# Kernel optimization log

Measured on AMD Instinct MI355X. Metric: run time of the kernel, lower is better.

## Reference

```python
import jax, jax.numpy as jnp
import numpy as np
from jax import lax

# ---- config (matches init_kwargs) ----
B, T, H = 4, 2048, 1024
HU = 4 * H                 # h_up = hidden*4
LAYERS, INDEX = 12, 0
K_CLAMP, K_EPS = 60.0, 1e-8
LN_EPS = 1e-5


def setup_inputs() -> dict:
    key = jax.random.key(0)
    ks = jax.random.split(key, 9)
    s = 0.02  # weight scale
    tr01 = INDEX / (LAYERS - 1)          # time_ratio_0_to_1
    tr1pz = 1.0 - INDEX / LAYERS         # time_ratio_1_to_pz
    i_h = np.arange(H, dtype=np.float64) / H
    i_hu = np.arange(HU, dtype=np.float64)
    # per-channel decay speed / first (sized to the WKV channel dim h_up)
    decay_speed = -5.0 + 8.0 * (i_hu / (HU - 1)) ** (0.7 + 1.3 * tr01)
    zigzag = ((np.arange(HU) + 1) % 3 - 1) * 0.5
    time_first = np.log(0.3) + zigzag
    f32 = lambda a: jnp.asarray(a, jnp.float32)
    return {
        "x": jax.random.normal(ks[0], (B, T, H), jnp.float32),
        "ln0_g": jnp.ones((H,), jnp.float32), "ln0_b": jnp.zeros((H,), jnp.float32),
        "pre_g": jnp.ones((H,), jnp.float32), "pre_b": jnp.zeros((H,), jnp.float32),
        "post_g": jnp.ones((H,), jnp.float32), "post_b": jnp.zeros((H,), jnp.float32),
        "tm_decay": f32(decay_speed),
        "tm_first": f32(time_first),
        "tm_mix_k": f32(i_h ** tr1pz),
        "tm_mix_v": f32(i_h ** tr1pz + 0.3 * tr01),
        "tm_mix_r": f32(i_h ** (0.5 * tr1pz)),
        "tm_Wk": jax.random.normal(ks[1], (H, HU), jnp.float32) * s,
        "tm_Wv": jax.random.normal(ks[2], (H, HU), jnp.float32) * s,
        "tm_Wr": jax.random.normal(ks[3], (H, HU), jnp.float32) * s,
        "tm_Wo": jax.random.normal(ks[4], (HU, H), jnp.float32) * s,
        "cm_mix_k": f32(i_h ** tr1pz),
        "cm_mix_r": f32(i_h ** tr1pz),
        "cm_Wk": jax.random.normal(ks[5], (H, HU), jnp.float32) * s,
        "cm_Wv": jax.random.normal(ks[6], (HU, H), jnp.float32) * s,
        "cm_Wr": jax.random.normal(ks[7], (H, H), jnp.float32) * s,
    }


def _ln(x, g, b):
    m = jnp.mean(x, -1, keepdims=True)
    v = jnp.mean((x - m) ** 2, -1, keepdims=True)
    return (x - m) / jnp.sqrt(v + LN_EPS) * g + b


def _shift(x):  # ZeroPad2d((0,0,1,-1)): xx[:, t] = x[:, t-1], xx[:, 0] = 0
    return jnp.pad(x[:, :-1], ((0, 0), (1, 0), (0, 0)))


def _wkv(k, kv, decay, first):
    # k, kv: [B, T, HU]; decay, first: [HU]
    # wkv[t] = first*kv[t] + sum_{d>=1} decay^(d-1) * kv[t-d]  (same for k)
    def step(carry, inp):
        sk, skv = carry
        kt, kvt = inp
        out = (first * kt + sk, first * kvt + skv)
        return (kt + decay * sk, kvt + decay * skv), out
    b = k.shape[0]
    init = (jnp.zeros((b, k.shape[2]), k.dtype), jnp.zeros((b, k.shape[2]), k.dtype))
    _, (wk, wkv) = lax.scan(step, init, (jnp.swapaxes(k, 0, 1), jnp.swapaxes(kv, 0, 1)))
    return jnp.swapaxes(wk, 0, 1), jnp.swapaxes(wkv, 0, 1)


def reference(x, ln0_g, ln0_b, pre_g, pre_b, post_g, post_b,
              tm_decay, tm_first, tm_mix_k, tm_mix_v, tm_mix_r,
              tm_Wk, tm_Wv, tm_Wr, tm_Wo,
              cm_mix_k, cm_mix_r, cm_Wk, cm_Wv, cm_Wr):
    if INDEX == 0:
        x = _ln(x, ln0_g, ln0_b)

    # ---- RWKV_TM (time mix / WKV) ----
    xn = _ln(x, pre_g, pre_b)
    xx = _shift(xn)
    xk = xn * tm_mix_k + xx * (1.0 - tm_mix_k)
    xv = xn * tm_mix_v + xx * (1.0 - tm_mix_v)
    xr = xn * tm_mix_r + xx * (1.0 - tm_mix_r)
    k = jnp.exp(jnp.minimum(xk @ tm_Wk, K_CLAMP))   # [B,T,HU]
    v = xv @ tm_Wv                                  # [B,T,HU]
    r = xr @ tm_Wr                                  # [B,T,HU]
    kv = k * v
    decay = jnp.exp(-jnp.exp(tm_decay))  # per-step multiplier exp(-exp(time_decay))
    first = jnp.exp(tm_first)
    wk, wkv = _wkv(k, kv, decay, first)
    rwkv = jax.nn.sigmoid(r) * (wkv / (wk + K_EPS))
    x = x + rwkv @ tm_Wo

    # ---- RWKV_CM (channel mix) ----
    xn = _ln(x, post_g, post_b)
    xx = _shift(xn)
    xk = xn * cm_mix_k + xx * (1.0 - cm_mix_k)
    xr = xn * cm_mix_r + xx * (1.0 - cm_mix_r)
    kv = jax.nn.silu(xk @ cm_Wk) @ cm_Wv            # [B,T,H]
    x = x + (jax.nn.sigmoid(xr @ cm_Wr) + kv)
    return x
```

## Files before the change

### kernel.cpp

```cpp
#include <hip/hip_runtime.h>

#define Hdim  1024
#define Tdim  2048
#define Bdim  4
#define HUdim 4096
#define Mrows (Bdim*Tdim)
#define CHUNK 2048
#define NCH   (HUdim/CHUNK)
#define NSEG  16
#define SEGL  (Tdim/NSEG)
#define SCHUNK 16

typedef __bf16 bf16;
typedef __bf16 bf16x2 __attribute__((ext_vector_type(2)));
typedef __bf16 bf16x8 __attribute__((ext_vector_type(8)));
typedef float  floatx4 __attribute__((ext_vector_type(4)));

__device__ __forceinline__ bf16 f2bf(float x) { return (bf16)x; }

__global__ __launch_bounds__(256) void wconv_all(
    const float* __restrict__ s0, const float* __restrict__ s1, const float* __restrict__ s2,
    const float* __restrict__ s3, const float* __restrict__ s4, const float* __restrict__ s5,
    const float* __restrict__ s6,
    bf16* d0, bf16* d1, bf16* d2, bf16* d3, bf16* d4, bf16* d5, bf16* d6) {
  __shared__ float tile[64][65];
  int bid = blockIdx.x;
  const float* src; bf16* dst; int K, N, local;
  if (bid < 1024)      { src = s0; dst = d0; K = Hdim;  N = HUdim; local = bid; }
  else if (bid < 2048) { src = s1; dst = d1; K = Hdim;  N = HUdim; local = bid - 1024; }
  else if (bid < 3072) { src = s2; dst = d2; K = Hdim;  N = HUdim; local = bid - 2048; }
  else if (bid < 4096) { src = s3; dst = d3; K = HUdim; N = Hdim;  local = bid - 3072; }
  else if (bid < 5120) { src = s4; dst = d4; K = Hdim;  N = HUdim; local = bid - 4096; }
  else if (bid < 6144) { src = s5; dst = d5; K = HUdim; N = Hdim;  local = bid - 5120; }
  else                 { src = s6; dst = d6; K = Hdim;  N = Hdim;  local = bid - 6144; }
  const int nt = N >> 6;
  const int n0 = (local % nt) * 64, k0 = (local / nt) * 64;
  const int tr = threadIdx.x >> 6;
  const int tc = threadIdx.x & 63;
#pragma unroll
  for (int j = 0; j < 16; j++) {
    int r = j * 4 + tr;
    tile[r][tc] = src[(size_t)(k0 + r) * N + n0 + tc];
  }
  __syncthreads();
#pragma unroll
  for (int j = 0; j < 16; j++) {
    int r = j * 4 + tr;
    dst[(size_t)(n0 + r) * K + k0 + tc] = f2bf(tile[tc][r]);
  }
}

__device__ __forceinline__ void block_reduce4(float v[4], float* sm) {
#pragma unroll
  for (int off = 32; off > 0; off >>= 1) {
#pragma unroll
    for (int i = 0; i < 4; i++) v[i] += __shfl_down(v[i], off, 64);
  }
  const int w = threadIdx.x >> 6;
  if ((threadIdx.x & 63) == 0) {
#pragma unroll
    for (int i = 0; i < 4; i++) sm[w * 4 + i] = v[i];
  }
  __syncthreads();
#pragma unroll
  for (int i = 0; i < 4; i++) v[i] = sm[i] + sm[4 + i] + sm[8 + i] + sm[12 + i];
  __syncthreads();
}

__global__ __launch_bounds__(256) void ln_mix_tm(
    const float* __restrict__ x,
    const float* __restrict__ g0, const float* __restrict__ b0,
    const float* __restrict__ g1, const float* __restrict__ b1,
    const float* __restrict__ mk, const float* __restrict__ mv, const float* __restrict__ mr,
    float* __restrict__ x0, bf16* __restrict__ xk, bf16* __restrict__ xv, bf16* __restrict__ xr) {
  __shared__ float sm[16];
  const int bid = blockIdx.x;
  const int t = bid & (Tdim - 1);
  const int tid = threadIdx.x;
  const bool havep = (t > 0);
  const float hp = havep ? 1.f : 0.f;
  const float* rowc = x + (size_t)bid * Hdim;
  const float* rowp = havep ? (rowc - Hdim) : rowc;

  float c[4], p[4];
#pragma unroll
  for (int j = 0; j < 4; j++) c[j] = rowc[tid * 4 + j];
#pragma unroll
  for (int j = 0; j < 4; j++) p[j] = rowp[tid * 4 + j] * hp;

  float red[4] = {0.f, 0.f, 0.f, 0.f};
#pragma unroll
  for (int j = 0; j < 4; j++) { red[0] += c[j]; red[1] += c[j]*c[j]; red[2] += p[j]; red[3] += p[j]*p[j]; }
  block_reduce4(red, sm);
  const float inv = 1.f / Hdim;
  float mc = red[0]*inv, vc = red[1]*inv - mc*mc;
  float mp = red[2]*inv, vp = red[3]*inv - mp*mp;
  float sc = rsqrtf(vc + 1e-5f), sp = rsqrtf(vp + 1e-5f);

  float yc[4], yp[4];
#pragma unroll
  for (int j = 0; j < 4; j++) {
    int i = tid * 4 + j;
    yc[j] = (c[j] - mc) * sc * g0[i] + b0[i];
    yp[j] = ((p[j] - mp) * sp * g0[i] + b0[i]) * hp;
    x0[(size_t)bid * Hdim + i] = yc[j];
  }

  float r2[4] = {0.f, 0.f, 0.f, 0.f};
#pragma unroll
  for (int j = 0; j < 4; j++) { r2[0] += yc[j]; r2[1] += yc[j]*yc[j]; r2[2] += yp[j]; r2[3] += yp[j]*yp[j]; }
  block_reduce4(r2, sm);
  float mc2 = r2[0]*inv, vc2 = r2[1]*inv - mc2*mc2;
  float mp2 = r2[2]*inv, vp2 = r2[3]*inv - mp2*mp2;
  float sc2 = rsqrtf(vc2 + 1e-5f), sp2 = rsqrtf(vp2 + 1e-5f);

#pragma unroll
  for (int j = 0; j < 4; j++) {
    int i = tid * 4 + j;
    float xnc = (yc[j] - mc2) * sc2 * g1[i] + b1[i];
    float xnp = ((yp[j] - mp2) * sp2 * g1[i] + b1[i]) * hp;
    size_t o = (size_t)bid * Hdim + i;
    float a;
    a = mk[i]; xk[o] = f2bf(xnc * a + xnp * (1.f - a));
    a = mv[i]; xv[o] = f2bf(xnc * a + xnp * (1.f - a));
    a = mr[i]; xr[o] = f2bf(xnc * a + xnp * (1.f - a));
  }
}

__global__ __launch_bounds__(256) void ln_mix_cm(
    const float* __restrict__ xin,
    const float* __restrict__ g, const float* __restrict__ bb,
    const float* __restrict__ mk, const float* __restrict__ mr,
    bf16* __restrict__ xk, bf16* __restrict__ xr) {
  __shared__ float sm[16];
  const int bid = blockIdx.x;
  const int t = bid & (Tdim - 1);
  const int tid = threadIdx.x;
  const bool havep = (t > 0);
  const float hp = havep ? 1.f : 0.f;
  const float* rowc = xin + (size_t)bid * Hdim;
  const float* rowp = havep ? (rowc - Hdim) : rowc;

  float c[4], p[4];
#pragma unroll
  for (int j = 0; j < 4; j++) c[j] = rowc[tid * 4 + j];
#pragma unroll
  for (int j = 0; j < 4; j++) p[j] = rowp[tid * 4 + j] * hp;

  float red[4] = {0.f, 0.f, 0.f, 0.f};
#pragma unroll
  for (int j = 0; j < 4; j++) { red[0] += c[j]; red[1] += c[j]*c[j]; red[2] += p[j]; red[3] += p[j]*p[j]; }
  block_reduce4(red, sm);
  const float inv = 1.f / Hdim;
  float mc = red[0]*inv, vc = red[1]*inv - mc*mc;
  float mp = red[2]*inv, vp = red[3]*inv - mp*mp;
  float sc = rsqrtf(vc + 1e-5f), sp = rsqrtf(vp + 1e-5f);

#pragma unroll
  for (int j = 0; j < 4; j++) {
    int i = tid * 4 + j;
    float xnc = (c[j] - mc) * sc * g[i] + bb[i];
    float xnp = ((p[j] - mp) * sp * g[i] + bb[i]) * hp;
    size_t o = (size_t)bid * Hdim + i;
    float a;
    a = mk[i]; xk[o] = f2bf(xnc * a + xnp * (1.f - a));
    a = mr[i]; xr[o] = f2bf(xnc * a + xnp * (1.f - a));
  }
}

__global__ __launch_bounds__(64) void wkv_part(
    const bf16* __restrict__ Kb, const bf16* __restrict__ Vb,
    float* __restrict__ stK, float* __restrict__ stKV,
    const float* __restrict__ tdec) {
  const int seg = blockIdx.x & (NSEG - 1);
  const int rest = blockIdx.x >> 4;
  const int b = rest >> 4, g = rest & 15;
  const int c = (g << 7) + (threadIdx.x << 1);
  const float d0 = __expf(-__expf(tdec[c]));
  const float d1 = __expf(-__expf(tdec[c + 1]));
  size_t base = ((size_t)b * Tdim + (size_t)seg * SEGL) * CHUNK + c;
  float sk0 = 0.f, skv0 = 0.f, sk1 = 0.f, skv1 = 0.f;
  for (int t0 = 0; t0 < SEGL; t0 += SCHUNK) {
    bf16x2 kk[SCHUNK], vv[SCHUNK];
#pragma unroll
    for (int j = 0; j < SCHUNK; j++) {
      size_t idx = base + (size_t)(t0 + j) * CHUNK;
      kk[j] = *(const bf16x2*)(Kb + idx);
      vv[j] = *(const bf16x2*)(Vb + idx);
    }
#pragma unroll
    for (int j = 0; j < SCHUNK; j++) {
      float k0 = (float)kk[j][0], k1 = (float)kk[j][1];
      float v0 = (float)vv[j][0], v1 = (float)vv[j][1];
      sk0  = fmaf(d0, sk0, k0);   skv0 = fmaf(d0, skv0, k0 * v0);
      sk1  = fmaf(d1, sk1, k1);   skv1 = fmaf(d1, skv1, k1 * v1);
    }
  }
  size_t so = ((size_t)seg * Bdim + b) * CHUNK + c;
  stK[so]      = sk0;  stK[so + 1]  = sk1;
  stKV[so]     = skv0; stKV[so + 1] = skv1;
}

__global__ __launch_bounds__(64) void wkv_emit(
    const bf16* __restrict__ Kb, const bf16* __restrict__ Vb,
    const bf16* SRb, bf16* Pb,
    const float* __restrict__ stK, const float* __restrict__ stKV,
    const float* __restrict__ tdec, const float* __restrict__ tfst) {
  const int seg = blockIdx.x & (NSEG - 1);
  const int rest = blockIdx.x >> 4;
  const int b = rest >> 4, g = rest & 15;
  const int c = (g << 7) + (threadIdx.x << 1);
  const float ed0 = __expf(tdec[c]),     ed1 = __expf(tdec[c + 1]);
  const float d0  = __expf(-ed0),        d1  = __expf(-ed1);
  const float df0 = __expf(-ed0 * (float)SEGL);
  const float df1 = __expf(-ed1 * (float)SEGL);
  const float f0  = __expf(tfst[c]),     f1  = __expf(tfst[c + 1]);

  float sk0 = 0.f, skv0 = 0.f, sk1 = 0.f, skv1 = 0.f;
  for (int j = 0; j < seg; j++) {
    size_t so = ((size_t)j * Bdim + b) * CHUNK + c;
    sk0  = fmaf(df0, sk0,  stK[so]);      sk1  = fmaf(df1, sk1,  stK[so + 1]);
    skv0 = fmaf(df0, skv0, stKV[so]);     skv1 = fmaf(df1, skv1, stKV[so + 1]);
  }

  size_t base = ((size_t)b * Tdim + (size_t)seg * SEGL) * CHUNK + c;
  for (int t0 = 0; t0 < SEGL; t0 += SCHUNK) {
    bf16x2 kk[SCHUNK], vv[SCHUNK], rr[SCHUNK];
#pragma unroll
    for (int j = 0; j < SCHUNK; j++) {
      size_t idx = base + (size_t)(t0 + j) * CHUNK;
      kk[j] = *(const bf16x2*)(Kb + idx);
      vv[j] = *(const bf16x2*)(Vb + idx);
      rr[j] = *(const bf16x2*)(SRb + idx);
    }
#pragma unroll
    for (int j = 0; j < SCHUNK; j++) {
      size_t idx = base + (size_t)(t0 + j) * CHUNK;
      float k0 = (float)kk[j][0], k1 = (float)kk[j][1];
      float v0 = (float)vv[j][0], v1 = (float)vv[j][1];
      float kv0 = k0 * v0, kv1 = k1 * v1;
      float wk0  = fmaf(f0, k0, sk0) + 1e-8f;
      float wk1  = fmaf(f1, k1, sk1) + 1e-8f;
      float wkv0 = fmaf(f0, kv0, skv0);
      float wkv1 = fmaf(f1, kv1, skv1);
      bf16x2 out;
      out[0] = f2bf((float)rr[j][0] * wkv0 * __builtin_amdgcn_rcpf(wk0));
      out[1] = f2bf((float)rr[j][1] * wkv1 * __builtin_amdgcn_rcpf(wk1));
      *(bf16x2*)(Pb + idx) = out;
      sk0  = fmaf(d0, sk0, k0);   skv0 = fmaf(d0, skv0, kv0);
      sk1  = fmaf(d1, sk1, k1);   skv1 = fmaf(d1, skv1, kv1);
    }
  }
}

__device__ __forceinline__ void gld_lds(const bf16* g, bf16* l) {
  __builtin_amdgcn_global_load_lds(
      (const __attribute__((address_space(1))) void*)(g),
      (__attribute__((address_space(3))) void*)(l),
      16, 0, 0);
}

__device__ __forceinline__ void swz(int s, int gm, int& m_t, int& n_t) {
  const int mpx  = gm >> 3;
  const int xcd  = s & 7;
  const int ss   = s >> 3;
  const int pass = mpx << 1;
  const int ng   = ss / pass;
  const int rem  = ss - ng * pass;
  m_t = xcd * mpx + (rem >> 1);
  n_t = (ng << 1) + (rem & 1);
}

__device__ __forceinline__ void mm_core64(
    const bf16* A, const bf16* Bt, int lda, int ldb, int K,
    long m0, long n0, int wv, int lane, int wm, int wn,
    bf16* As, bf16* Bs, floatx4 acc[4][4]) {
  const int srow = wv * 32 + (lane >> 2);
  const int scol = (((lane & 3) - ((lane >> 3) & 3)) & 3) * 8;
  const bf16* gA = A + (m0 + srow) * (long)lda + scol;
  const bf16* gB = Bt + (n0 + srow) * (long)ldb + scol;
  const long skipA = 16L * lda;
  const long skipB = 16L * ldb;
  bf16* lA = As + wv * 1024;
  bf16* lB = Bs + wv * 1024;
  const int pg = ((lane >> 4) + ((lane >> 1) & 3)) & 3;
  const bf16* fa = As + ((wm * 64) + (lane & 15)) * 32 + pg * 8;
  const bf16* fb = Bs + ((wn * 64) + (lane & 15)) * 32 + pg * 8;

  const int ksteps = K >> 6;
  for (int kt = 0; kt < ksteps; ++kt) {
    __syncthreads();
    gld_lds(gA, lA);             gld_lds(gA + skipA, lA + 512);
    gld_lds(gA + 32, lA + 4096); gld_lds(gA + 32 + skipA, lA + 4096 + 512);
    gld_lds(gB, lB);             gld_lds(gB + skipB, lB + 512);
    gld_lds(gB + 32, lB + 4096); gld_lds(gB + 32 + skipB, lB + 4096 + 512);
    gA += 64; gB += 64;
    __syncthreads();
#pragma unroll
    for (int s = 0; s < 2; s++) {
      bf16x8 af[4], bfr[4];
#pragma unroll
      for (int i = 0; i < 4; i++) {
        af[i]  = *(const bf16x8*)(fa + s * 4096 + i * 512);
        bfr[i] = *(const bf16x8*)(fb + s * 4096 + i * 512);
      }
#pragma unroll
      for (int mt = 0; mt < 4; mt++)
#pragma unroll
        for (int nt = 0; nt < 4; nt++)
          acc[mt][nt] = __builtin_amdgcn_mfma_f32_16x16x32_bf16(af[mt], bfr[nt], acc[mt][nt], 0, 0, 0);
    }
  }
}

enum { E_EXP = 0, E_BF16 = 1, E_SIG = 2, E_ADD1 = 3, E_SILU = 4, E_F32 = 5, E_SIGADD2 = 6 };

template <int EPI>
__device__ __forceinline__ void epilogue(
    floatx4 acc[4][4], void* Cout, const void* aux1, const void* aux2,
    long m0, long n0, int ldc, int lane, int wm, int wn) {
  const int r0 = wm * 64 + ((lane >> 4) << 2);
  const int c0 = wn * 64 + (lane & 15);
#pragma unroll
  for (int mt = 0; mt < 4; mt++) {
#pragma unroll
    for (int i = 0; i < 4; i++) {
      long r = m0 + r0 + mt * 16 + i;
      long bidx = r * (long)ldc + n0 + c0;
#pragma unroll
      for (int nt = 0; nt < 4; nt++) {
        long idx = bidx + nt * 16;
        float v = acc[mt][nt][i];
        if constexpr (EPI == E_EXP) {
          ((bf16*)Cout)[idx] = f2bf(__expf(fminf(v, 60.f)));
        } else if constexpr (EPI == E_BF16) {
          ((bf16*)Cout)[idx] = f2bf(v);
        } else if constexpr (EPI == E_SIG) {
          ((bf16*)Cout)[idx] = f2bf(1.f / (1.f + __expf(-v)));
        } else if constexpr (EPI == E_ADD1) {
          float prev = ((const float*)aux1)[idx];
          ((float*)Cout)[idx] = v + prev;
        } else if constexpr (EPI == E_SILU) {
          ((bf16*)Cout)[idx] = f2bf(v / (1.f + __expf(-v)));
        } else if constexpr (EPI == E_F32) {
          ((float*)Cout)[idx] = v;
        } else {
          float a1 = ((const float*)aux1)[idx];
          float a2 = ((const float*)aux2)[idx];
          ((float*)Cout)[idx] = a1 + 1.f / (1.f + __expf(-v)) + a2;
        }
      }
    }
  }
}

template <int EPI, int MT>
__global__ __launch_bounds__(256) void gemm_bt(
    const bf16* __restrict__ A, const bf16* __restrict__ Bt,
    void* Cout, const void* aux1, const void* aux2,
    int lda, int ldb, int ldc, int K, int gm, int gn) {
  __shared__ __align__(16) bf16 As[2 * 128 * 32];
  __shared__ __align__(16) bf16 Bs[2 * 128 * 32];
  const int tid = threadIdx.x;
  const int lane = tid & 63;
  const int wv = tid >> 6;
  const int wm = wv >> 1, wn = wv & 1;
  int m_t, n_t;
  swz(blockIdx.x, gm, m_t, n_t);
  const long n0 = (long)n_t * 128;

#pragma unroll
  for (int sm = 0; sm < MT; sm++) {
    const long m0 = (long)m_t * (128 * MT) + sm * 128;
    floatx4 acc[4][4];
#pragma unroll
    for (int i = 0; i < 4; i++)
#pragma unroll
      for (int j = 0; j < 4; j++) acc[i][j] = (floatx4){0.f, 0.f, 0.f, 0.f};
    mm_core64(A, Bt, lda, ldb, K, m0, n0, wv, lane, wm, wn, As, Bs, acc);
    epilogue<EPI>(acc, Cout, aux1, aux2, m0, n0, ldc, lane, wm, wn);
  }
}

__global__ __launch_bounds__(256) void proj3(
    const bf16* __restrict__ xk, const bf16* __restrict__ xv, const bf16* __restrict__ xr,
    const bf16* __restrict__ Wk, const bf16* __restrict__ Wv, const bf16* __restrict__ Wr,
    bf16* Kc, bf16* Vc, bf16* SRc, int gm, int gn) {
  __shared__ __align__(16) bf16 As[2 * 128 * 32];
  __shared__ __align__(16) bf16 Bs[2 * 128 * 32];
  const int per = gm * gn;
  const int sub = blockIdx.x / per;
  const int s   = blockIdx.x - sub * per;
  const int tid = threadIdx.x;
  const int lane = tid & 63;
  const int wv = tid >> 6;
  const int wm = wv >> 1, wn = wv & 1;
  int m_t, n_t;
  swz(s, gm, m_t, n_t);
  const long n0 = (long)n_t * 128;

  const bf16* A  = (sub == 0) ? xk : (sub == 1) ? xv : xr;
  const bf16* Bt = (sub == 0) ? Wk : (sub == 1) ? Wv : Wr;
  bf16*       C  = (sub == 0) ? Kc : (sub == 1) ? Vc : SRc;

#pragma unroll
  for (int sm = 0; sm < 2; sm++) {
    const long m0 = (long)m_t * 256 + sm * 128;
    floatx4 acc[4][4];
#pragma unroll
    for (int i = 0; i < 4; i++)
#pragma unroll
      for (int j = 0; j < 4; j++) acc[i][j] = (floatx4){0.f, 0.f, 0.f, 0.f};
    mm_core64(A, Bt, Hdim, Hdim, Hdim, m0, n0, wv, lane, wm, wn, As, Bs, acc);

    const int r0 = wm * 64 + ((lane >> 4) << 2);
    const int c0 = wn * 64 + (lane & 15);
#pragma unroll
    for (int mt = 0; mt < 4; mt++) {
#pragma unroll
      for (int i = 0; i < 4; i++) {
        long r = m0 + r0 + mt * 16 + i;
        long bidx = r * (long)CHUNK + n0 + c0;
#pragma unroll
        for (int nt = 0; nt < 4; nt++) {
          long idx = bidx + nt * 16;
          float v = acc[mt][nt][i];
          float o;
          if (sub == 0)      o = __expf(fminf(v, 60.f));
          else if (sub == 1) o = v;
          else               o = 1.f / (1.f + __expf(-v));
          C[idx] = f2bf(o);
        }
      }
    }
  }
}

extern "C" void kernel_launch(void* const* d_in, const int* in_sizes, int n_in,
                              void* d_out, int out_size, void* d_ws, size_t ws_size,
                              hipStream_t stream) {
  (void)in_sizes; (void)n_in; (void)out_size; (void)ws_size;
  const float* x        = (const float*)d_in[0];
  const float* ln0_g    = (const float*)d_in[1];
  const float* ln0_b    = (const float*)d_in[2];
  const float* pre_g    = (const float*)d_in[3];
  const float* pre_b    = (const float*)d_in[4];
  const float* post_g   = (const float*)d_in[5];
  const float* post_b   = (const float*)d_in[6];
  const float* tm_decay = (const float*)d_in[7];
  const float* tm_first = (const float*)d_in[8];
  const float* tm_mix_k = (const float*)d_in[9];
  const float* tm_mix_v = (const float*)d_in[10];
  const float* tm_mix_r = (const float*)d_in[11];
  const float* tm_Wk    = (const float*)d_in[12];
  const float* tm_Wv    = (const float*)d_in[13];
  const float* tm_Wr    = (const float*)d_in[14];
  const float* tm_Wo    = (const float*)d_in[15];
  const float* cm_mix_k = (const float*)d_in[16];
  const float* cm_mix_r = (const float*)d_in[17];
  const float* cm_Wk    = (const float*)d_in[18];
  const float* cm_Wv    = (const float*)d_in[19];
  const float* cm_Wr    = (const float*)d_in[20];

  char* ws = (char*)d_ws;
  bf16*  WkT  = (bf16*)(ws + 0);
  bf16*  WvT  = (bf16*)(ws + 8388608);
  bf16*  WrT  = (bf16*)(ws + 16777216);
  bf16*  WoT  = (bf16*)(ws + 25165824);
  bf16*  cWkT = (bf16*)(ws + 33554432);
  bf16*  cWvT = (bf16*)(ws + 41943040);
  bf16*  cWrT = (bf16*)(ws + 50331648);
  float* xres = (float*)(ws + 52428800);
  bf16*  xk   = (bf16*)(ws + 85983232);
  bf16*  xv   = (bf16*)(ws + 102760448);
  bf16*  xr   = (bf16*)(ws + 119537664);
  bf16*  Kc   = (bf16*)(ws + 136314880);
  bf16*  Vc   = (bf16*)(ws + 169869312);
  bf16*  SRc  = (bf16*)(ws + 203423744);
  float* stK  = (float*)(ws + 236978176);
  float* stKV = (float*)(ws + 237502464);
  bf16*  xk2  = (bf16*)(ws + 136314880);
  bf16*  xr2  = (bf16*)(ws + 153092096);
  bf16*  hbuf = (bf16*)(ws + 169869312);
  float* hv   = (float*)(ws + 85983232);

  dim3 blk(256);
  wconv_all<<<6400, blk, 0, stream>>>(tm_Wk, tm_Wv, tm_Wr, tm_Wo, cm_Wk, cm_Wv, cm_Wr,
                                      WkT, WvT, WrT, WoT, cWkT, cWvT, cWrT);

  ln_mix_tm<<<Mrows, blk, 0, stream>>>(x, ln0_g, ln0_b, pre_g, pre_b,
                                       tm_mix_k, tm_mix_v, tm_mix_r, xres, xk, xv, xr);

  const int scan_grid = NSEG * Bdim * (CHUNK / 128);
  const int GM = Mrows / 128;
  const int GM2 = Mrows / 256;
  const int GNp = CHUNK / 128;
  for (int ch = 0; ch < NCH; ch++) {
    const long woff = (long)ch * CHUNK;
    proj3<<<3 * GM2 * GNp, blk, 0, stream>>>(
        xk, xv, xr, WkT + woff * Hdim, WvT + woff * Hdim, WrT + woff * Hdim,
        Kc, Vc, SRc, GM2, GNp);

    wkv_part<<<scan_grid, dim3(64), 0, stream>>>(
        Kc, Vc, stK, stKV, tm_decay + woff);
    wkv_emit<<<scan_grid, dim3(64), 0, stream>>>(
        Kc, Vc, SRc, SRc, stK, stKV, tm_decay + woff, tm_first + woff);

    gemm_bt<E_ADD1, 1><<<GM * (Hdim/128), blk, 0, stream>>>(
        SRc, WoT + woff, xres, xres, nullptr, CHUNK, HUdim, Hdim, CHUNK, GM, Hdim/128);
  }

  ln_mix_cm<<<Mrows, blk, 0, stream>>>(xres, post_g, post_b, cm_mix_k, cm_mix_r, xk2, xr2);

  gemm_bt<E_SILU, 2><<<GM2 * (HUdim/128), blk, 0, stream>>>(
      xk2, cWkT, hbuf, nullptr, nullptr, Hdim, Hdim, HUdim, Hdim, GM2, HUdim/128);

  gemm_bt<E_F32, 1><<<GM * (Hdim/128), blk, 0, stream>>>(
      hbuf, cWvT, hv, nullptr, nullptr, HUdim, HUdim, Hdim, CHUNK, GM, Hdim/128);
  gemm_bt<E_ADD1, 1><<<GM * (Hdim/128), blk, 0, stream>>>(
      hbuf + CHUNK, cWvT + CHUNK, hv, hv, nullptr, HUdim, HUdim, Hdim, CHUNK, GM, Hdim/128);

  gemm_bt<E_SIGADD2, 1><<<GM * (Hdim/128), blk, 0, stream>>>(
      xr2, cWrT, (float*)d_out, xres, hv, Hdim, Hdim, Hdim, Hdim, GM, Hdim/128);
}
```

Measured before the change: 988.2 us.

## Use 256x256 eight-wave MFMA GEMM tiles for projections and channel-mix up-proj

Adds a 512-thread GEMM core that computes a 256x256 output tile per block. It uses 128-deep K stages double-buffered in LDS via direct global-to-LDS loads, with phased barriers and setprio around the MFMA bursts. The time-mix projection kernel and the channel-mix SiLU up-projection now use this core in place of the 128-wide, 4-wave tiles. Larger tiles raise arithmetic intensity and cut global and LDS traffic per FLOP, at the cost of higher register and LDS use (128KB LDS per block) and fewer blocks for load balancing.

```diff
diff --git a/kernel.cpp b/kernel.cpp
--- a/kernel.cpp
+++ b/kernel.cpp
@@ -382,55 +382,187 @@
   }
 }
 
-__global__ __launch_bounds__(256) void proj3(
+__device__ __forceinline__ void mm_core256(
+    const bf16* __restrict__ A, const bf16* __restrict__ Bt,
+    int lda, int ldb, int K, long m0, long n0,
+    int wv, int lane, bf16* Lds, floatx4 acc[8][4]) {
+  const int wm = wv >> 2, wn = wv & 3;
+  const int rA0 = wm * 128 + (wv & 3) * 16;
+  const int rB0 = (wv >> 1) * 64 + (wv & 1) * 16;
+  const int rl  = lane >> 2;
+  const int scol = (((lane & 3) - ((lane >> 3) & 3)) & 3) * 8;
+  const bf16* gA = A + (m0 + rA0 + rl) * (long)lda + scol;
+  const bf16* gB = Bt + (n0 + rB0 + rl) * (long)ldb + scol;
+  bf16* lA = Lds + rA0 * 32;
+  bf16* lB = Lds + 16384 + rB0 * 32;
+
+  const int pg = ((lane >> 4) + ((lane >> 1) & 3)) & 3;
+  const bf16* fa0 = Lds + (wm * 128 + (lane & 15)) * 32 + pg * 8;
+  const bf16* fb0 = Lds + 16384 + (wn * 64 + (lane & 15)) * 32 + pg * 8;
+
+#define STGA8(buf, h, kt) do { \
+    const bf16* _s = gA + (long)(h) * 64 * lda + (kt) * 64; \
+    bf16* _d = lA + (buf) * 32768 + (h) * 2048; \
+    gld_lds(_s, _d); gld_lds(_s + 32, _d + 8192); } while (0)
+#define STGB8(buf, h, kt) do { \
+    const bf16* _s = gB + (long)(h) * 32 * ldb + (kt) * 64; \
+    bf16* _d = lB + (buf) * 32768 + (h) * 1024; \
+    gld_lds(_s, _d); gld_lds(_s + 32, _d + 8192); } while (0)
+
+  STGA8(0, 0, 0); STGA8(0, 1, 0); STGB8(0, 0, 0); STGB8(0, 1, 0);
+  STGA8(1, 0, 1); STGB8(1, 0, 1);
+  asm volatile("s_waitcnt vmcnt(4)" ::: "memory");
+  __builtin_amdgcn_s_barrier();
+
+  const int niter = K >> 7;
+  for (int it = 0; it < niter; ++it) {
+    const int kt0 = it << 1;
+    const bool notlast = (it != niter - 1);
+#pragma unroll
+    for (int ph = 0; ph < 8; ++ph) {
+      const int buf = ph >> 2;
+      const int mq = (ph >> 1) & 1, nq = ph & 1;
+      bf16x8 a[4][2], b[2][2];
+      const bf16* fa = fa0 + buf * 32768 + mq * 2048;
+      const bf16* fb = fb0 + buf * 32768 + nq * 1024;
+#pragma unroll
+      for (int mf = 0; mf < 4; ++mf) {
+        a[mf][0] = *(const bf16x8*)(fa + mf * 512);
+        a[mf][1] = *(const bf16x8*)(fa + mf * 512 + 8192);
+      }
+#pragma unroll
+      for (int nf = 0; nf < 2; ++nf) {
+        b[nf][0] = *(const bf16x8*)(fb + nf * 512);
+        b[nf][1] = *(const bf16x8*)(fb + nf * 512 + 8192);
+      }
+      __builtin_amdgcn_sched_barrier(0);
+      if (ph == 0)      STGA8(1, 1, kt0 + 1);
+      else if (ph == 1) STGB8(1, 1, kt0 + 1);
+      else if (notlast) {
+        if (ph == 2)      STGA8(0, 0, kt0 + 2);
+        else if (ph == 3) STGB8(0, 0, kt0 + 2);
+        else if (ph == 4) STGA8(0, 1, kt0 + 2);
+        else if (ph == 5) STGB8(0, 1, kt0 + 2);
+        else if (ph == 6) STGA8(1, 0, kt0 + 3);
+        else              STGB8(1, 0, kt0 + 3);
+      }
+      if (ph == 3) {
+        if (notlast) { asm volatile("s_waitcnt vmcnt(4)" ::: "memory"); }
+        else         { asm volatile("s_waitcnt vmcnt(0)" ::: "memory"); }
+      } else if (ph == 7 && notlast) {
+        asm volatile("s_waitcnt vmcnt(4)" ::: "memory");
+      }
+      __builtin_amdgcn_s_barrier();
+      asm volatile("s_waitcnt lgkmcnt(0)" ::: "memory");
+      __builtin_amdgcn_s_setprio(1);
+#pragma unroll
+      for (int mf = 0; mf < 4; ++mf)
+#pragma unroll
+        for (int nf = 0; nf < 2; ++nf) {
+          acc[mq*4+mf][nq*2+nf] = __builtin_amdgcn_mfma_f32_16x16x32_bf16(
+              a[mf][0], b[nf][0], acc[mq*4+mf][nq*2+nf], 0, 0, 0);
+          acc[mq*4+mf][nq*2+nf] = __builtin_amdgcn_mfma_f32_16x16x32_bf16(
+              a[mf][1], b[nf][1], acc[mq*4+mf][nq*2+nf], 0, 0, 0);
+        }
+      __builtin_amdgcn_s_setprio(0);
+      __builtin_amdgcn_s_barrier();
+    }
+  }
+#undef STGA8
+#undef STGB8
+}
+
+template <int EPI>
+__global__ __launch_bounds__(512, 2) void gemm8(
+    const bf16* __restrict__ A, const bf16* __restrict__ Bt,
+    void* Cout, const void* aux1, const void* aux2,
+    int lda, int ldb, int ldc, int K, int gm, int gn) {
+  __shared__ __align__(16) bf16 Lds[65536];
+  const int tid = threadIdx.x;
+  const int lane = tid & 63;
+  const int wv = tid >> 6;
+  int m_t, n_t;
+  swz(blockIdx.x, gm, m_t, n_t);
+  const long m0 = (long)m_t * 256, n0 = (long)n_t * 256;
+  floatx4 acc[8][4];
+#pragma unroll
+  for (int i = 0; i < 8; i++)
+#pragma unroll
+    for (int j = 0; j < 4; j++) acc[i][j] = (floatx4){0.f, 0.f, 0.f, 0.f};
+  mm_core256(A, Bt, lda, ldb, K, m0, n0, wv, lane, Lds, acc);
+
+  const int wm = wv >> 2, wn = wv & 3;
+  const int r0 = wm * 128 + ((lane >> 4) << 2);
+  const int c0 = wn * 64 + (lane & 15);
+#pragma unroll
+  for (int mf = 0; mf < 8; ++mf) {
+#pragma unroll
+    for (int i = 0; i < 4; ++i) {
+      long r = m0 + r0 + mf * 16 + i;
+      long bidx = r * (long)ldc + n0 + c0;
+#pragma unroll
+      for (int nf = 0; nf < 4; ++nf) {
+        long idx = bidx + nf * 16;
+        float v = acc[mf][nf][i];
+        if constexpr (EPI == E_SILU) {
+          ((bf16*)Cout)[idx] = f2bf(v / (1.f + __expf(-v)));
+        } else if constexpr (EPI == E_BF16) {
+          ((bf16*)Cout)[idx] = f2bf(v);
+        } else if constexpr (EPI == E_F32) {
+          ((float*)Cout)[idx] = v;
+        } else if constexpr (EPI == E_ADD1) {
+          float prev = ((const float*)aux1)[idx];
+          ((float*)Cout)[idx] = v + prev;
+        }
+      }
+    }
+  }
+}
+
+__global__ __launch_bounds__(512, 2) void proj8(
     const bf16* __restrict__ xk, const bf16* __restrict__ xv, const bf16* __restrict__ xr,
     const bf16* __restrict__ Wk, const bf16* __restrict__ Wv, const bf16* __restrict__ Wr,
     bf16* Kc, bf16* Vc, bf16* SRc, int gm, int gn) {
-  __shared__ __align__(16) bf16 As[2 * 128 * 32];
-  __shared__ __align__(16) bf16 Bs[2 * 128 * 32];
+  __shared__ __align__(16) bf16 Lds[65536];
   const int per = gm * gn;
   const int sub = blockIdx.x / per;
   const int s   = blockIdx.x - sub * per;
   const int tid = threadIdx.x;
   const int lane = tid & 63;
   const int wv = tid >> 6;
-  const int wm = wv >> 1, wn = wv & 1;
   int m_t, n_t;
   swz(s, gm, m_t, n_t);
-  const long n0 = (long)n_t * 128;
+  const long m0 = (long)m_t * 256, n0 = (long)n_t * 256;
 
   const bf16* A  = (sub == 0) ? xk : (sub == 1) ? xv : xr;
   const bf16* Bt = (sub == 0) ? Wk : (sub == 1) ? Wv : Wr;
   bf16*       C  = (sub == 0) ? Kc : (sub == 1) ? Vc : SRc;
 
-#pragma unroll
-  for (int sm = 0; sm < 2; sm++) {
-    const long m0 = (long)m_t * 256 + sm * 128;
-    floatx4 acc[4][4];
-#pragma unroll
-    for (int i = 0; i < 4; i++)
-#pragma unroll
-      for (int j = 0; j < 4; j++) acc[i][j] = (floatx4){0.f, 0.f, 0.f, 0.f};
-    mm_core64(A, Bt, Hdim, Hdim, Hdim, m0, n0, wv, lane, wm, wn, As, Bs, acc);
-
-    const int r0 = wm * 64 + ((lane >> 4) << 2);
-    const int c0 = wn * 64 + (lane & 15);
-#pragma unroll
-    for (int mt = 0; mt < 4; mt++) {
-#pragma unroll
-      for (int i = 0; i < 4; i++) {
-        long r = m0 + r0 + mt * 16 + i;
-        long bidx = r * (long)CHUNK + n0 + c0;
-#pragma unroll
-        for (int nt = 0; nt < 4; nt++) {
-          long idx = bidx + nt * 16;
-          float v = acc[mt][nt][i];
-          float o;
-          if (sub == 0)      o = __expf(fminf(v, 60.f));
-          else if (sub == 1) o = v;
-          else               o = 1.f / (1.f + __expf(-v));
-          C[idx] = f2bf(o);
-        }
+  floatx4 acc[8][4];
+#pragma unroll
+  for (int i = 0; i < 8; i++)
+#pragma unroll
+    for (int j = 0; j < 4; j++) acc[i][j] = (floatx4){0.f, 0.f, 0.f, 0.f};
+  mm_core256(A, Bt, Hdim, Hdim, Hdim, m0, n0, wv, lane, Lds, acc);
+
+  const int wm = wv >> 2, wn = wv & 3;
+  const int r0 = wm * 128 + ((lane >> 4) << 2);
+  const int c0 = wn * 64 + (lane & 15);
+#pragma unroll
+  for (int mf = 0; mf < 8; ++mf) {
+#pragma unroll
+    for (int i = 0; i < 4; ++i) {
+      long r = m0 + r0 + mf * 16 + i;
+      long bidx = r * (long)CHUNK + n0 + c0;
+#pragma unroll
+      for (int nf = 0; nf < 4; ++nf) {
+        long idx = bidx + nf * 16;
+        float v = acc[mf][nf][i];
+        float o;
+        if (sub == 0)      o = __expf(fminf(v, 60.f));
+        else if (sub == 1) o = v;
+        else               o = 1.f / (1.f + __expf(-v));
+        C[idx] = f2bf(o);
       }
     }
   }
@@ -493,13 +625,13 @@
 
   const int scan_grid = NSEG * Bdim * (CHUNK / 128);
   const int GM = Mrows / 128;
-  const int GM2 = Mrows / 256;
-  const int GNp = CHUNK / 128;
+  const int GM8 = Mrows / 256;
+  const int GN8p = CHUNK / 256;
   for (int ch = 0; ch < NCH; ch++) {
     const long woff = (long)ch * CHUNK;
-    proj3<<<3 * GM2 * GNp, blk, 0, stream>>>(
+    proj8<<<3 * GM8 * GN8p, dim3(512), 0, stream>>>(
         xk, xv, xr, WkT + woff * Hdim, WvT + woff * Hdim, WrT + woff * Hdim,
-        Kc, Vc, SRc, GM2, GNp);
+        Kc, Vc, SRc, GM8, GN8p);
 
     wkv_part<<<scan_grid, dim3(64), 0, stream>>>(
         Kc, Vc, stK, stKV, tm_decay + woff);
@@ -512,8 +644,8 @@
 
   ln_mix_cm<<<Mrows, blk, 0, stream>>>(xres, post_g, post_b, cm_mix_k, cm_mix_r, xk2, xr2);
 
-  gemm_bt<E_SILU, 2><<<GM2 * (HUdim/128), blk, 0, stream>>>(
-      xk2, cWkT, hbuf, nullptr, nullptr, Hdim, Hdim, HUdim, Hdim, GM2, HUdim/128);
+  gemm8<E_SILU><<<GM8 * (HUdim/256), dim3(512), 0, stream>>>(
+      xk2, cWkT, hbuf, nullptr, nullptr, Hdim, Hdim, HUdim, Hdim, GM8, HUdim/256);
 
   gemm_bt<E_F32, 1><<<GM * (Hdim/128), blk, 0, stream>>>(
       hbuf, cWvT, hv, nullptr, nullptr, HUdim, HUdim, Hdim, CHUNK, GM, Hdim/128);
```

Result: faster. 926.5 us (-6.2%).

## Replace GEMM core with 8-wave triple-buffered pipelined 256x128 tile kernel

Applied to the files above, without the earlier changes.

Replaces the 4-wave, single-buffered 128x128 GEMM main loop with an 8-wave (512-thread) kernel computing 256x128 tiles. Global-to-LDS loads are staged two k-steps ahead in a triple-buffered LDS ring, with vmcnt waits, s_setprio around the MFMA bursts and a single barrier per iteration, so loads overlap compute. All projection and channel-mix GEMMs switch to the new kernel, and the split-K pair for cm_Wv is merged into one full-K GEMM. The larger LDS footprint and 2-blocks-per-CU launch bound trade occupancy and register headroom for more tile reuse.

```diff
diff --git a/kernel.cpp b/kernel.cpp
--- a/kernel.cpp
+++ b/kernel.cpp
@@ -269,48 +269,6 @@
   const int rem  = ss - ng * pass;
   m_t = xcd * mpx + (rem >> 1);
   n_t = (ng << 1) + (rem & 1);
-}
-
-__device__ __forceinline__ void mm_core64(
-    const bf16* A, const bf16* Bt, int lda, int ldb, int K,
-    long m0, long n0, int wv, int lane, int wm, int wn,
-    bf16* As, bf16* Bs, floatx4 acc[4][4]) {
-  const int srow = wv * 32 + (lane >> 2);
-  const int scol = (((lane & 3) - ((lane >> 3) & 3)) & 3) * 8;
-  const bf16* gA = A + (m0 + srow) * (long)lda + scol;
-  const bf16* gB = Bt + (n0 + srow) * (long)ldb + scol;
-  const long skipA = 16L * lda;
-  const long skipB = 16L * ldb;
-  bf16* lA = As + wv * 1024;
-  bf16* lB = Bs + wv * 1024;
-  const int pg = ((lane >> 4) + ((lane >> 1) & 3)) & 3;
-  const bf16* fa = As + ((wm * 64) + (lane & 15)) * 32 + pg * 8;
-  const bf16* fb = Bs + ((wn * 64) + (lane & 15)) * 32 + pg * 8;
-
-  const int ksteps = K >> 6;
-  for (int kt = 0; kt < ksteps; ++kt) {
-    __syncthreads();
-    gld_lds(gA, lA);             gld_lds(gA + skipA, lA + 512);
-    gld_lds(gA + 32, lA + 4096); gld_lds(gA + 32 + skipA, lA + 4096 + 512);
-    gld_lds(gB, lB);             gld_lds(gB + skipB, lB + 512);
-    gld_lds(gB + 32, lB + 4096); gld_lds(gB + 32 + skipB, lB + 4096 + 512);
-    gA += 64; gB += 64;
-    __syncthreads();
-#pragma unroll
-    for (int s = 0; s < 2; s++) {
-      bf16x8 af[4], bfr[4];
-#pragma unroll
-      for (int i = 0; i < 4; i++) {
-        af[i]  = *(const bf16x8*)(fa + s * 4096 + i * 512);
-        bfr[i] = *(const bf16x8*)(fb + s * 4096 + i * 512);
-      }
-#pragma unroll
-      for (int mt = 0; mt < 4; mt++)
-#pragma unroll
-        for (int nt = 0; nt < 4; nt++)
-          acc[mt][nt] = __builtin_amdgcn_mfma_f32_16x16x32_bf16(af[mt], bfr[nt], acc[mt][nt], 0, 0, 0);
-    }
-  }
 }
 
 enum { E_EXP = 0, E_BF16 = 1, E_SIG = 2, E_ADD1 = 3, E_SILU = 4, E_F32 = 5, E_SIGADD2 = 6 };
@@ -354,83 +312,147 @@
   }
 }
 
-template <int EPI, int MT>
-__global__ __launch_bounds__(256) void gemm_bt(
+__device__ __forceinline__ void mm_core_n128(
+    const bf16* __restrict__ A, const bf16* __restrict__ Bt,
+    int lda, int ldb, int K, long m0, long n0,
+    int wv, int lane, bf16* Lds, floatx4 acc[4][4]) {
+  const int rl  = lane >> 2;
+  const int scol = (((lane & 3) - ((lane >> 3) & 3)) & 3) * 8;
+  const bf16* gA = A + (m0 + wv * 16 + rl) * (long)lda + scol;
+  const bf16* gB = Bt + (n0 + wv * 16 + rl) * (long)ldb + scol;
+  bf16* lA = Lds + wv * 512;
+  bf16* lB = Lds + 49152 + wv * 512;
+
+  const int wm = wv >> 1, wn = wv & 1;
+  const int pg = ((lane >> 4) + ((lane >> 1) & 3)) & 3;
+  const bf16* fa0 = Lds + (wm * 64 + (lane & 15)) * 32 + pg * 8;
+  const bf16* fb0 = Lds + 49152 + (wn * 64 + (lane & 15)) * 32 + pg * 8;
+
+#define STGA_N(buf, h, kt) do { \
+    const bf16* _s = gA + (long)(h) * 128 * lda + (long)(kt) * 64; \
+    bf16* _d = lA + (buf) * 16384 + (h) * 4096; \
+    gld_lds(_s, _d); gld_lds(_s + 32, _d + 8192); } while (0)
+#define STGB_N(buf, kt) do { \
+    const bf16* _s = gB + (long)(kt) * 64; \
+    bf16* _d = lB + (buf) * 8192; \
+    gld_lds(_s, _d); gld_lds(_s + 32, _d + 4096); } while (0)
+
+  STGA_N(0, 0, 0); STGA_N(0, 1, 0); STGB_N(0, 0);
+  STGA_N(1, 0, 1); STGA_N(1, 1, 1); STGB_N(1, 1);
+  asm volatile("s_waitcnt vmcnt(6)" ::: "memory");
+  __builtin_amdgcn_s_barrier();
+
+  const int niter = K >> 6;
+  int p = 0;
+  for (int it = 0; it < niter; ++it) {
+    const int q = (p >= 1) ? p - 1 : p + 2;
+    const bool dostage = (it <= niter - 3);
+    const bf16* fa = fa0 + p * 16384;
+    const bf16* fb = fb0 + p * 8192;
+
+    bf16x8 a0[4], b0v[4], a1[4], b1v[4];
+#pragma unroll
+    for (int i = 0; i < 4; ++i) {
+      a0[i]  = *(const bf16x8*)(fa + i * 512);
+      b0v[i] = *(const bf16x8*)(fb + i * 512);
+    }
+#pragma unroll
+    for (int i = 0; i < 4; ++i) {
+      a1[i]  = *(const bf16x8*)(fa + 8192 + i * 512);
+      b1v[i] = *(const bf16x8*)(fb + 4096 + i * 512);
+    }
+    __builtin_amdgcn_sched_barrier(0);
+    if (dostage) { STGA_N(q, 0, it + 2); STGA_N(q, 1, it + 2); STGB_N(q, it + 2); }
+    __builtin_amdgcn_s_setprio(1);
+#pragma unroll
+    for (int mf = 0; mf < 4; ++mf)
+#pragma unroll
+      for (int nf = 0; nf < 4; ++nf)
+        acc[mf][nf] = __builtin_amdgcn_mfma_f32_16x16x32_bf16(a0[mf], b0v[nf], acc[mf][nf], 0, 0, 0);
+#pragma unroll
+    for (int mf = 0; mf < 4; ++mf)
+#pragma unroll
+      for (int nf = 0; nf < 4; ++nf)
+        acc[mf][nf] = __builtin_amdgcn_mfma_f32_16x16x32_bf16(a1[mf], b1v[nf], acc[mf][nf], 0, 0, 0);
+    __builtin_amdgcn_s_setprio(0);
+
+    if (it < niter - 1) {
+      if (dostage) asm volatile("s_waitcnt vmcnt(6)" ::: "memory");
+      else         asm volatile("s_waitcnt vmcnt(0)" ::: "memory");
+      __builtin_amdgcn_s_barrier();
+    }
+    p = (p == 2) ? 0 : p + 1;
+  }
+#undef STGA_N
+#undef STGB_N
+}
+
+template <int EPI>
+__global__ __launch_bounds__(512, 2) void gemm8n(
     const bf16* __restrict__ A, const bf16* __restrict__ Bt,
     void* Cout, const void* aux1, const void* aux2,
     int lda, int ldb, int ldc, int K, int gm, int gn) {
-  __shared__ __align__(16) bf16 As[2 * 128 * 32];
-  __shared__ __align__(16) bf16 Bs[2 * 128 * 32];
+  __shared__ __align__(16) bf16 Lds[73728];
   const int tid = threadIdx.x;
   const int lane = tid & 63;
   const int wv = tid >> 6;
-  const int wm = wv >> 1, wn = wv & 1;
   int m_t, n_t;
   swz(blockIdx.x, gm, m_t, n_t);
-  const long n0 = (long)n_t * 128;
-
-#pragma unroll
-  for (int sm = 0; sm < MT; sm++) {
-    const long m0 = (long)m_t * (128 * MT) + sm * 128;
-    floatx4 acc[4][4];
-#pragma unroll
-    for (int i = 0; i < 4; i++)
-#pragma unroll
-      for (int j = 0; j < 4; j++) acc[i][j] = (floatx4){0.f, 0.f, 0.f, 0.f};
-    mm_core64(A, Bt, lda, ldb, K, m0, n0, wv, lane, wm, wn, As, Bs, acc);
-    epilogue<EPI>(acc, Cout, aux1, aux2, m0, n0, ldc, lane, wm, wn);
-  }
-}
-
-__global__ __launch_bounds__(256) void proj3(
+  const long m0 = (long)m_t * 256, n0 = (long)n_t * 128;
+  floatx4 acc[4][4];
+#pragma unroll
+  for (int i = 0; i < 4; i++)
+#pragma unroll
+    for (int j = 0; j < 4; j++) acc[i][j] = (floatx4){0.f, 0.f, 0.f, 0.f};
+  mm_core_n128(A, Bt, lda, ldb, K, m0, n0, wv, lane, Lds, acc);
+  const int wm = wv >> 1, wn = wv & 1;
+  epilogue<EPI>(acc, Cout, aux1, aux2, m0, n0, ldc, lane, wm, wn);
+}
+
+__global__ __launch_bounds__(512, 2) void proj8n(
     const bf16* __restrict__ xk, const bf16* __restrict__ xv, const bf16* __restrict__ xr,
     const bf16* __restrict__ Wk, const bf16* __restrict__ Wv, const bf16* __restrict__ Wr,
     bf16* Kc, bf16* Vc, bf16* SRc, int gm, int gn) {
-  __shared__ __align__(16) bf16 As[2 * 128 * 32];
-  __shared__ __align__(16) bf16 Bs[2 * 128 * 32];
+  __shared__ __align__(16) bf16 Lds[73728];
   const int per = gm * gn;
   const int sub = blockIdx.x / per;
   const int s   = blockIdx.x - sub * per;
   const int tid = threadIdx.x;
   const int lane = tid & 63;
   const int wv = tid >> 6;
-  const int wm = wv >> 1, wn = wv & 1;
   int m_t, n_t;
   swz(s, gm, m_t, n_t);
-  const long n0 = (long)n_t * 128;
+  const long m0 = (long)m_t * 256, n0 = (long)n_t * 128;
 
   const bf16* A  = (sub == 0) ? xk : (sub == 1) ? xv : xr;
   const bf16* Bt = (sub == 0) ? Wk : (sub == 1) ? Wv : Wr;
   bf16*       C  = (sub == 0) ? Kc : (sub == 1) ? Vc : SRc;
 
-#pragma unroll
-  for (int sm = 0; sm < 2; sm++) {
-    const long m0 = (long)m_t * 256 + sm * 128;
-    floatx4 acc[4][4];
-#pragma unroll
-    for (int i = 0; i < 4; i++)
-#pragma unroll
-      for (int j = 0; j < 4; j++) acc[i][j] = (floatx4){0.f, 0.f, 0.f, 0.f};
-    mm_core64(A, Bt, Hdim, Hdim, Hdim, m0, n0, wv, lane, wm, wn, As, Bs, acc);
-
-    const int r0 = wm * 64 + ((lane >> 4) << 2);
-    const int c0 = wn * 64 + (lane & 15);
-#pragma unroll
-    for (int mt = 0; mt < 4; mt++) {
-#pragma unroll
-      for (int i = 0; i < 4; i++) {
-        long r = m0 + r0 + mt * 16 + i;
-        long bidx = r * (long)CHUNK + n0 + c0;
-#pragma unroll
-        for (int nt = 0; nt < 4; nt++) {
-          long idx = bidx + nt * 16;
-          float v = acc[mt][nt][i];
-          float o;
-          if (sub == 0)      o = __expf(fminf(v, 60.f));
-          else if (sub == 1) o = v;
-          else               o = 1.f / (1.f + __expf(-v));
-          C[idx] = f2bf(o);
-        }
+  floatx4 acc[4][4];
+#pragma unroll
+  for (int i = 0; i < 4; i++)
+#pragma unroll
+    for (int j = 0; j < 4; j++) acc[i][j] = (floatx4){0.f, 0.f, 0.f, 0.f};
+  mm_core_n128(A, Bt, Hdim, Hdim, Hdim, m0, n0, wv, lane, Lds, acc);
+
+  const int wm = wv >> 1, wn = wv & 1;
+  const int r0 = wm * 64 + ((lane >> 4) << 2);
+  const int c0 = wn * 64 + (lane & 15);
+#pragma unroll
+  for (int mt = 0; mt < 4; ++mt) {
+#pragma unroll
+    for (int i = 0; i < 4; ++i) {
+      long r = m0 + r0 + mt * 16 + i;
+      long bidx = r * (long)CHUNK + n0 + c0;
+#pragma unroll
+      for (int nt = 0; nt < 4; ++nt) {
+        long idx = bidx + nt * 16;
+        float v = acc[mt][nt][i];
+        float o;
+        if (sub == 0)      o = __expf(fminf(v, 60.f));
+        else if (sub == 1) o = v;
+        else               o = 1.f / (1.f + __expf(-v));
+        C[idx] = f2bf(o);
       }
     }
   }
@@ -492,34 +514,32 @@
                                        tm_mix_k, tm_mix_v, tm_mix_r, xres, xk, xv, xr);
 
   const int scan_grid = NSEG * Bdim * (CHUNK / 128);
-  const int GM = Mrows / 128;
-  const int GM2 = Mrows / 256;
+  const int GM8 = Mrows / 256;
   const int GNp = CHUNK / 128;
+  const int GNn = Hdim / 128;
   for (int ch = 0; ch < NCH; ch++) {
     const long woff = (long)ch * CHUNK;
-    proj3<<<3 * GM2 * GNp, blk, 0, stream>>>(
+    proj8n<<<3 * GM8 * GNp, dim3(512), 0, stream>>>(
         xk, xv, xr, WkT + woff * Hdim, WvT + woff * Hdim, WrT + woff * Hdim,
-        Kc, Vc, SRc, GM2, GNp);
+        Kc, Vc, SRc, GM8, GNp);
 
     wkv_part<<<scan_grid, dim3(64), 0, stream>>>(
         Kc, Vc, stK, stKV, tm_decay + woff);
     wkv_emit<<<scan_grid, dim3(64), 0, stream>>>(
         Kc, Vc, SRc, SRc, stK, stKV, tm_decay + woff, tm_first + woff);
 
-    gemm_bt<E_ADD1, 1><<<GM * (Hdim/128), blk, 0, stream>>>(
-        SRc, WoT + woff, xres, xres, nullptr, CHUNK, HUdim, Hdim, CHUNK, GM, Hdim/128);
+    gemm8n<E_ADD1><<<GM8 * GNn, dim3(512), 0, stream>>>(
+        SRc, WoT + woff, xres, xres, nullptr, CHUNK, HUdim, Hdim, CHUNK, GM8, GNn);
   }
 
   ln_mix_cm<<<Mrows, blk, 0, stream>>>(xres, post_g, post_b, cm_mix_k, cm_mix_r, xk2, xr2);
 
-  gemm_bt<E_SILU, 2><<<GM2 * (HUdim/128), blk, 0, stream>>>(
-      xk2, cWkT, hbuf, nullptr, nullptr, Hdim, Hdim, HUdim, Hdim, GM2, HUdim/128);
-
-  gemm_bt<E_F32, 1><<<GM * (Hdim/128), blk, 0, stream>>>(
-      hbuf, cWvT, hv, nullptr, nullptr, HUdim, HUdim, Hdim, CHUNK, GM, Hdim/128);
-  gemm_bt<E_ADD1, 1><<<GM * (Hdim/128), blk, 0, stream>>>(
-      hbuf + CHUNK, cWvT + CHUNK, hv, hv, nullptr, HUdim, HUdim, Hdim, CHUNK, GM, Hdim/128);
-
-  gemm_bt<E_SIGADD2, 1><<<GM * (Hdim/128), blk, 0, stream>>>(
-      xr2, cWrT, (float*)d_out, xres, hv, Hdim, Hdim, Hdim, Hdim, GM, Hdim/128);
-}
+  gemm8n<E_SILU><<<GM8 * (HUdim/128), dim3(512), 0, stream>>>(
+      xk2, cWkT, hbuf, nullptr, nullptr, Hdim, Hdim, HUdim, Hdim, GM8, HUdim/128);
+
+  gemm8n<E_F32><<<GM8 * GNn, dim3(512), 0, stream>>>(
+      hbuf, cWvT, hv, nullptr, nullptr, HUdim, HUdim, Hdim, HUdim, GM8, GNn);
+
+  gemm8n<E_SIGADD2><<<GM8 * GNn, dim3(512), 0, stream>>>(
+      xr2, cWrT, (float*)d_out, xres, hv, Hdim, Hdim, Hdim, Hdim, GM8, GNn);
+}
```

New measurement: 870.2 us. 1.14x faster.
